# Performance work log

Measured on AMD Instinct MI355X. Metric: run time of the kernel, lower is better.

## Reference

```python
import jax, jax.numpy as jnp
import numpy as np

# Hough voting constants from the call site:
# Hough(angle=90, R2_list=[4,64,256,1024], num_classes=1, region_num=13, vote_field_size=33)
ANGLE = 90
R2_LIST = (4, 64, 256, 1024)
REGION_NUM = 13
VFS = 33  # vote field size


def _hough_filter():
    """Log-polar vote-field filter [region_num, VFS, VFS].

    Region 0 = center disk (r^2 <= R2_LIST[0]); region 1 + ring*4 + angle_bin
    for the 3 radius rings x 4 angle sectors. Each region's weights are
    1/(#pixels in region) so each region's vote sums to 1 (HoughNet log map).
    """
    c = VFS // 2
    ys, xs = np.meshgrid(np.arange(VFS) - c, np.arange(VFS) - c, indexing='ij')
    r2 = xs ** 2 + ys ** 2
    theta = (np.degrees(np.arctan2(ys, xs)) + 360.0) % 360.0
    nang = 360 // ANGLE  # 4 angle sectors
    abin = np.minimum((theta // ANGLE).astype(np.int64), nang - 1)
    region = -np.ones((VFS, VFS), np.int64)
    region[r2 <= R2_LIST[0]] = 0
    for i in range(1, len(R2_LIST)):
        m = (r2 > R2_LIST[i - 1]) & (r2 <= R2_LIST[i])
        region[m] = 1 + (i - 1) * nang + abin[m]
    filt = np.zeros((REGION_NUM, VFS, VFS), np.float32)
    for r in range(REGION_NUM):
        m = region == r
        if m.sum() > 0:
            filt[r][m] = 1.0 / float(m.sum())
    return filt


# ConvTranspose2d(13 -> 1, k=33, stride=1, pad=16) == SAME conv with flipped kernel.
_HOUGH_CONV_W = jnp.asarray(np.flip(_hough_filter(), axis=(1, 2))[None].copy())  # [1,13,33,33]


def setup_inputs() -> dict:
    key = jax.random.key(0)
    ks = jax.random.split(key, 4)
    B, C, H, W = 2, 256, 256, 512
    return {
        'x': jax.random.normal(ks[0], (B, C, H, W), jnp.float32),
        'pos_w': jax.random.normal(ks[1], (13, C), jnp.float32) * 0.05,
        'pos_b': jnp.zeros((13,), jnp.float32),
        'reg_w': jax.random.normal(ks[2], (1, C), jnp.float32) * 0.05,
        'reg_b': jnp.zeros((1,), jnp.float32),
        'off_w': jax.random.normal(ks[3], (2, C), jnp.float32) * 0.05,
        'off_b': jnp.zeros((2,), jnp.float32),
    }


def _conv1x1(x, w, b):
    # x: [B,C,H,W], w: [O,C] -> [B,O,H,W]
    return jnp.einsum('bchw,oc->bohw', x, w) + b[None, :, None, None]


def reference(x, pos_w, pos_b, reg_w, reg_b, off_w, off_b):
    evident = jax.nn.relu(_conv1x1(x, pos_w, pos_b))  # [B,13,H,W]
    score = jax.lax.conv_general_dilated(
        evident, _HOUGH_CONV_W, (1, 1), 'SAME',
        dimension_numbers=('NCHW', 'OIHW', 'NCHW'))  # [B,1,H,W]
    x_cls = jax.nn.sigmoid(score)
    x_reg = _conv1x1(x, reg_w, reg_b)
    x_off = _conv1x1(x, off_w, off_b)
    return (x_cls, x_reg, x_off)
```

## Files before the change

kernel.cpp:

```cpp
#include <hip/hip_runtime.h>
#include <math.h>

#define BB   2
#define CC   256
#define HH   256
#define WW   512
#define HW   (HH*WW)
#define IMG  (CC*HW)

#define HPP  288
#define WPP  546
#define CHPP (HPP*WPP)
#define EVB2 (13*CHPP)
#define EV2_FLOATS (BB*EVB2)

#define OUT_REG (BB*HW)
#define OUT_OFF (2*BB*HW)

static __device__ __forceinline__ int region_of(int ys, int xs) {
    int r2 = ys * ys + xs * xs;
    int bin;
    if (ys == 0)     bin = (xs >= 0) ? 0 : 2;
    else if (ys > 0) bin = (xs > 0) ? 0 : 1;
    else             bin = (xs < 0) ? 2 : 3;
    if (r2 <= 4)   return 0;
    if (r2 <= 64)  return 1 + bin;
    if (r2 <= 256) return 5 + bin;
    return 9 + bin;
}

__global__ void setup_k(const float* __restrict__ pw, const float* __restrict__ pb,
                        const float* __restrict__ rw, const float* __restrict__ rb,
                        const float* __restrict__ ow, const float* __restrict__ ob,
                        float* __restrict__ wp, float* __restrict__ bias,
                        int2* __restrict__ tabg, int* __restrict__ mg,
                        float* __restrict__ ev) {
    int blk = blockIdx.x, tid = threadIdx.x;
    if (blk < 16) {
        int i = blk * 256 + tid;
        int c = i >> 4, o = i & 15;
        float v;
        if (o < 13)       v = pw[o * CC + c];
        else if (o == 13) v = rw[c];
        else              v = ow[(o - 14) * CC + c];
        wp[c * 16 + o] = v;
        if (i < 16) {
            float bv = (i < 13) ? pb[i] : (i == 13 ? rb[0] : ob[i - 14]);
            bias[i] = bv;
        }
    } else if (blk == 16) {
        __shared__ int cnt[13];
        __shared__ int runbuf[33 * 16];
        __shared__ int countrow[33];
        __shared__ int rowstart[34];
        if (tid < 13) cnt[tid] = 0;
        __syncthreads();
        for (int i = tid; i < 1089; i += 256) {
            int ky = i / 33, kx = i - ky * 33;
            atomicAdd(&cnt[region_of(16 - ky, 16 - kx)], 1);
        }
        __syncthreads();
        if (tid < 33) {
            int ky = tid, n = 0;
            int c0 = region_of(16 - ky, 16);
            int kxa = 0;
            for (int kx = 1; kx <= 33; kx++) {
                int c = (kx < 33) ? region_of(16 - ky, 16 - kx) : -1;
                if (c != c0) {
                    runbuf[tid * 16 + n] = c0 | (kxa << 4) | ((kx - 1) << 10);
                    n++;
                    c0 = c; kxa = kx;
                }
            }
            countrow[tid] = n;
        }
        __syncthreads();
        if (tid == 0) {
            int a = 0;
            for (int t = 0; t < 33; t++) { rowstart[t] = a; a += countrow[t]; }
            rowstart[33] = a;
            mg[0] = 2 * a;
        }
        __syncthreads();
        if (tid < 33) {
            int ky = tid, base = rowstart[tid], n = countrow[tid];
            for (int j = 0; j < n; j++) {
                int rn  = runbuf[tid * 16 + j];
                int c   = rn & 15, kxa = (rn >> 4) & 63, kxb = (rn >> 10) & 63;
                float w = 1.0f / (float)cnt[c];
                int off0 = c * CHPP + (ky - 16) * WPP;
                tabg[2 * (base + j)]     = make_int2(off0 + (kxb - 16), __float_as_int(w));
                tabg[2 * (base + j) + 1] = make_int2(off0 + (kxa - 17), __float_as_int(-w));
            }
        }
    } else {
        int seg   = blk - 17;
        int plane = seg >> 1;
        int half  = seg & 1;
        float* base = ev + (size_t)plane * CHPP + (half ? (size_t)272 * WPP : 0);
        float4 z = make_float4(0.f, 0.f, 0.f, 0.f);
        float4* b4 = (float4*)base;
#pragma unroll
        for (int it = 0; it < 9; it++) {
            int idx = it * 256 + tid;
            if (idx < 2184) b4[idx] = z;
        }
    }
}

__global__ __launch_bounds__(256) void convscan_k(
    const float* __restrict__ x, const float* __restrict__ wp,
    const float* __restrict__ bias, float* __restrict__ ev,
    float* __restrict__ out) {
    __shared__ float part[13][4];
    int tid  = threadIdx.x;
    int lane = tid & 63;
    int wv   = tid >> 6;
    int bid  = blockIdx.x;
    int b    = bid >> 8;
    int y    = bid & 255;
    int hw   = y * WW + tid * 2;
    const float* xb = x + (size_t)b * IMG + hw;

    float a0[16], a1[16];
#pragma unroll
    for (int o = 0; o < 16; o++) { a0[o] = 0.f; a1[o] = 0.f; }

#pragma unroll 4
    for (int c = 0; c < CC; c++) {
        float2 v = *(const float2*)(xb + c * HW);
        const float* wr = wp + c * 16;
#pragma unroll
        for (int o = 0; o < 16; o++) {
            float wv_ = wr[o];
            a0[o] = fmaf(v.x, wv_, a0[o]);
            a1[o] = fmaf(v.y, wv_, a1[o]);
        }
    }

#pragma unroll
    for (int o = 0; o < 13; o++) {
        float bo = bias[o];
        float e0 = fmaxf(a0[o] + bo, 0.f);
        float e1 = fmaxf(a1[o] + bo, 0.f);
        float s  = e0 + e1;
#pragma unroll
        for (int d = 1; d < 64; d <<= 1) {
            float t = __shfl_up(s, d, 64);
            if (lane >= d) s += t;
        }
        a0[o] = s - e1;
        a1[o] = s;
        if (lane == 63) part[o][wv] = s;
    }
    __syncthreads();

    size_t rowbase = (size_t)(b * 13) * CHPP + (size_t)(y + 16) * WPP;
#pragma unroll
    for (int o = 0; o < 13; o++) {
        float off = 0.f;
#pragma unroll
        for (int w2 = 0; w2 < 3; w2++)
            if (w2 < wv) off += part[o][w2];
        *(float2*)(&ev[rowbase + o * CHPP + 18 + tid * 2]) =
            make_float2(a0[o] + off, a1[o] + off);
    }
    if (tid < 234) {
        int o = tid / 18, j = tid - o * 18;
        ev[rowbase + o * CHPP + j] = 0.f;
    }
    if (tid < 208) {
        int o = tid >> 4, j = tid & 15;
        float tot = part[o][0] + part[o][1] + part[o][2] + part[o][3];
        ev[rowbase + o * CHPP + 530 + j] = tot;
    }

    *(float2*)(&out[OUT_REG + b * HW + hw]) =
        make_float2(a0[13] + bias[13], a1[13] + bias[13]);
    *(float2*)(&out[OUT_OFF + b * 2 * HW + hw]) =
        make_float2(a0[14] + bias[14], a1[14] + bias[14]);
    *(float2*)(&out[OUT_OFF + b * 2 * HW + HW + hw]) =
        make_float2(a0[15] + bias[15], a1[15] + bias[15]);
}

__global__ __launch_bounds__(256) void hough_k(const float* __restrict__ P,
                                               const int2* __restrict__ tabg,
                                               const int* __restrict__ mg,
                                               float* __restrict__ out) {
    int m   = mg[0];
    int tid = threadIdx.x;
    int bid = blockIdx.x;
    int sb  = (bid & 7) * 128 + (bid >> 3);
    int p   = sb * 256 + tid;
    int b   = p >> 17;
    int hw  = p & (HW - 1);
    int y   = hw >> 9, xx = hw & 511;
    const float* Pb = P + (size_t)b * EVB2 + (y + 16) * WPP + (xx + 18);

    float s = 0.f;
#pragma unroll 8
    for (int t = 0; t < m; t++) {
        int2 e = tabg[t];
        s = fmaf(Pb[e.x], __int_as_float(e.y), s);
    }
    out[b * HW + hw] = 1.0f / (1.0f + expf(-s));
}

extern "C" void kernel_launch(void* const* d_in, const int* in_sizes, int n_in,
                              void* d_out, int out_size, void* d_ws, size_t ws_size,
                              hipStream_t stream) {
    const float* x  = (const float*)d_in[0];
    const float* pw = (const float*)d_in[1];
    const float* pb = (const float*)d_in[2];
    const float* rw = (const float*)d_in[3];
    const float* rb = (const float*)d_in[4];
    const float* ow = (const float*)d_in[5];
    const float* ob = (const float*)d_in[6];
    float* out = (float*)d_out;

    float* ev   = (float*)d_ws;
    float* wp   = ev + EV2_FLOATS;
    float* bias = wp + 4096;
    int2*  tabg = (int2*)(bias + 16);
    int*   mg   = (int*)(tabg + 2048);

    setup_k<<<69, 256, 0, stream>>>(pw, pb, rw, rb, ow, ob, wp, bias, tabg, mg, ev);
    convscan_k<<<512, 256, 0, stream>>>(x, wp, bias, ev, out);
    hough_k<<<1024, 256, 0, stream>>>(ev, tabg, mg, out);
}
```

Baseline: 395.8 us.

## Fuse setup, conv-scan and Hough phases into one cooperative kernel

```diff
diff --git a/kernel.cpp b/kernel.cpp
--- a/kernel.cpp
+++ b/kernel.cpp
@@ -1,5 +1,8 @@
 #include <hip/hip_runtime.h>
+#include <hip/hip_cooperative_groups.h>
 #include <math.h>
+
+namespace cg = cooperative_groups;
 
 #define BB   2
 #define CC   256
@@ -29,13 +32,15 @@
     return 9 + bin;
 }
 
-__global__ void setup_k(const float* __restrict__ pw, const float* __restrict__ pb,
-                        const float* __restrict__ rw, const float* __restrict__ rb,
-                        const float* __restrict__ ow, const float* __restrict__ ob,
-                        float* __restrict__ wp, float* __restrict__ bias,
-                        int2* __restrict__ tabg, int* __restrict__ mg,
-                        float* __restrict__ ev) {
-    int blk = blockIdx.x, tid = threadIdx.x;
+static __device__ __forceinline__ void phase_setup(
+    int blk, int tid,
+    const float* __restrict__ pw, const float* __restrict__ pb,
+    const float* __restrict__ rw, const float* __restrict__ rb,
+    const float* __restrict__ ow, const float* __restrict__ ob,
+    float* __restrict__ wp, float* __restrict__ bias,
+    int2* __restrict__ tabg, int* __restrict__ mg,
+    float* __restrict__ ev)
+{
     if (blk < 16) {
         int i = blk * 256 + tid;
         int c = i >> 4, o = i & 15;
@@ -108,15 +113,15 @@
     }
 }
 
-__global__ __launch_bounds__(256) void convscan_k(
+static __device__ __forceinline__ void phase_conv(
+    int bid, int tid,
     const float* __restrict__ x, const float* __restrict__ wp,
     const float* __restrict__ bias, float* __restrict__ ev,
-    float* __restrict__ out) {
+    float* __restrict__ out)
+{
     __shared__ float part[13][4];
-    int tid  = threadIdx.x;
     int lane = tid & 63;
     int wv   = tid >> 6;
-    int bid  = blockIdx.x;
     int b    = bid >> 8;
     int y    = bid & 255;
     int hw   = y * WW + tid * 2;
@@ -181,6 +186,63 @@
         make_float2(a0[14] + bias[14], a1[14] + bias[14]);
     *(float2*)(&out[OUT_OFF + b * 2 * HW + HW + hw]) =
         make_float2(a0[15] + bias[15], a1[15] + bias[15]);
+}
+
+__global__ __launch_bounds__(256) void fused_k(
+    const float* __restrict__ x,
+    const float* __restrict__ pw, const float* __restrict__ pb,
+    const float* __restrict__ rw, const float* __restrict__ rb,
+    const float* __restrict__ ow, const float* __restrict__ ob,
+    float* __restrict__ wp, float* __restrict__ bias,
+    int2* __restrict__ tabg, int* __restrict__ mg,
+    float* __restrict__ ev, float* __restrict__ out)
+{
+    int tid = threadIdx.x;
+    int bid = blockIdx.x;
+
+    if (bid < 69)
+        phase_setup(bid, tid, pw, pb, rw, rb, ow, ob, wp, bias, tabg, mg, ev);
+    __threadfence();
+    cg::this_grid().sync();
+
+    phase_conv(bid, tid, x, wp, bias, ev, out);
+    __threadfence();
+    cg::this_grid().sync();
+
+    int m   = mg[0];
+    int sb  = (bid & 7) * 64 + (bid >> 3);
+    int p0  = sb * 512 + tid;
+    int b2  = p0 >> 17;
+    int hw2 = p0 & (HW - 1);
+    int y2  = hw2 >> 9, xx = hw2 & 511;
+    const float* Pb = ev + (size_t)b2 * EVB2 + (y2 + 16) * WPP + (xx + 18);
+
+    float s0 = 0.f, s1 = 0.f;
+#pragma unroll 4
+    for (int t = 0; t < m; t++) {
+        int2 e  = tabg[t];
+        float w = __int_as_float(e.y);
+        s0 = fmaf(Pb[e.x],       w, s0);
+        s1 = fmaf(Pb[e.x + 256], w, s1);
+    }
+    out[b2 * HW + hw2]       = 1.0f / (1.0f + expf(-s0));
+    out[b2 * HW + hw2 + 256] = 1.0f / (1.0f + expf(-s1));
+}
+
+__global__ void setup_k(const float* __restrict__ pw, const float* __restrict__ pb,
+                        const float* __restrict__ rw, const float* __restrict__ rb,
+                        const float* __restrict__ ow, const float* __restrict__ ob,
+                        float* __restrict__ wp, float* __restrict__ bias,
+                        int2* __restrict__ tabg, int* __restrict__ mg,
+                        float* __restrict__ ev) {
+    phase_setup(blockIdx.x, threadIdx.x, pw, pb, rw, rb, ow, ob, wp, bias, tabg, mg, ev);
+}
+
+__global__ __launch_bounds__(256) void convscan_k(
+    const float* __restrict__ x, const float* __restrict__ wp,
+    const float* __restrict__ bias, float* __restrict__ ev,
+    float* __restrict__ out) {
+    phase_conv(blockIdx.x, threadIdx.x, x, wp, bias, ev, out);
 }
 
 __global__ __launch_bounds__(256) void hough_k(const float* __restrict__ P,
@@ -224,7 +286,17 @@
     int2*  tabg = (int2*)(bias + 16);
     int*   mg   = (int*)(tabg + 2048);
 
-    setup_k<<<69, 256, 0, stream>>>(pw, pb, rw, rb, ow, ob, wp, bias, tabg, mg, ev);
-    convscan_k<<<512, 256, 0, stream>>>(x, wp, bias, ev, out);
-    hough_k<<<1024, 256, 0, stream>>>(ev, tabg, mg, out);
-}
+    void* kargs[] = {
+        (void*)&x, (void*)&pw, (void*)&pb, (void*)&rw, (void*)&rb,
+        (void*)&ow, (void*)&ob, (void*)&wp, (void*)&bias, (void*)&tabg,
+        (void*)&mg, (void*)&ev, (void*)&out
+    };
+    hipError_t err = hipLaunchCooperativeKernel(
+        reinterpret_cast<void*>(fused_k), dim3(512), dim3(256), kargs, 0, stream);
+    if (err != hipSuccess) {
+        (void)hipGetLastError();
+        setup_k<<<69, 256, 0, stream>>>(pw, pb, rw, rb, ow, ob, wp, bias, tabg, mg, ev);
+        convscan_k<<<512, 256, 0, stream>>>(x, wp, bias, ev, out);
+        hough_k<<<1024, 256, 0, stream>>>(ev, tabg, mg, out);
+    }
+}
```

After: 678.1 us. 1.71x slower.
